# Optimization experiments

Measured on AMD Instinct MI355X. Metric: run time of the kernel, lower is better.

## Reference

```python
import jax, jax.numpy as jnp
import numpy as np

N_USERS = 100000
N_ITEMS = 50000
N_TOPICS = 1000
N_NODES = N_USERS + N_ITEMS + N_TOPICS
DIM = 64
LAYERS = 3
NNZ = 4000000
BATCH = 16384


def setup_inputs() -> dict:
    key = jax.random.key(0)
    ks = jax.random.split(key, 8)
    user_w = jax.random.normal(ks[0], (N_USERS, DIM), dtype=jnp.float32) * 0.1
    item_w = jax.random.normal(ks[1], (N_ITEMS, DIM), dtype=jnp.float32) * 0.1
    topic_w = jax.random.normal(ks[2], (N_TOPICS, DIM), dtype=jnp.float32) * 0.1
    vals = jax.random.uniform(ks[3], (NNZ,), dtype=jnp.float32)
    row = jax.random.randint(ks[4], (NNZ,), 0, N_NODES, dtype=jnp.int32)
    col = jax.random.randint(ks[5], (NNZ,), 0, N_NODES, dtype=jnp.int32)
    users = jax.random.randint(ks[6], (BATCH,), 0, N_USERS, dtype=jnp.int32)
    items = jax.random.randint(ks[7], (BATCH,), 0, N_ITEMS, dtype=jnp.int32)
    return {"user_w": user_w, "item_w": item_w, "topic_w": topic_w,
            "vals": vals, "row": row, "col": col,
            "users": users, "items": items}


def _spmm(vals, row, col, x):
    # y[r] = sum over edges e with row[e]==r of vals[e] * x[col[e]]
    msgs = vals[:, None] * x[col]  # [NNZ, DIM]
    return jax.ops.segment_sum(msgs, row, num_segments=N_NODES)


def reference(user_w, item_w, topic_w, vals, row, col, users, items):
    all_emb = jnp.concatenate([user_w, item_w, topic_w], axis=0)  # [N, D]
    acc = all_emb
    emb = all_emb
    for _ in range(LAYERS):
        emb = _spmm(vals, row, col, emb)
        acc = acc + emb
    out = acc / jnp.asarray(LAYERS + 1, dtype=acc.dtype)  # mean over stacked layers
    u = out[users]                       # [B, D] user rows
    i = out[N_USERS + items]             # [B, D] item rows (offset into node table)
    return jnp.sum(u * i, axis=1)        # [B]
```

## Files before the change

kernel.cpp:

```cpp
#include <hip/hip_runtime.h>
#include <hip/hip_fp16.h>

#define N_USERS 100000
#define N_ITEMS 50000
#define N_TOPICS 1000
#define N_NODES (N_USERS + N_ITEMS + N_TOPICS)
#define DIM 64
#define NNZ 4000000
#define BATCH 16384

#define BROWS 128
#define NB ((N_NODES + BROWS - 1) / BROWS)
#define NPART 256
#define CHUNK ((NNZ + NPART - 1) / NPART)
#define SUB 7813
#define SEGCAP 4608

#define QSCALE 16384.0f
#define QINV   6.103515625e-05f

#define CONCAT_TOTAL (N_NODES * (DIM / 4))
#define CONCAT_BLOCKS ((CONCAT_TOTAL + 1023) / 1024)
#define BINIT_TOTAL (2 * BATCH * (DIM / 4))
#define BINIT_BLOCKS ((BINIT_TOTAL + 1023) / 1024)

__global__ void __launch_bounds__(1024)
phase0(const float4* __restrict__ uw,
       const float4* __restrict__ iw,
       const float4* __restrict__ tw,
       const int* __restrict__ row,
       const int* __restrict__ users,
       const int* __restrict__ items,
       __half2* __restrict__ x0,
       float4* __restrict__ accb,
       int* __restrict__ hcnt,
       int* __restrict__ sync) {
    __shared__ int h[NB];
    const int blk = blockIdx.x;
    const int t = threadIdx.x;
    if (blk < NPART) {
        if (blk == 0 && t == 0) *sync = 0;
        for (int i = t; i < NB; i += 1024) h[i] = 0;
        __syncthreads();
        int e0 = blk * CHUNK;
        int e1 = e0 + CHUNK; if (e1 > NNZ) e1 = NNZ;
        for (int e = e0 + t; e < e1; e += 1024) {
            int r = __builtin_nontemporal_load(&row[e]);
            atomicAdd(&h[r >> 7], 1);
        }
        __syncthreads();
        int* dst = hcnt + (size_t)blk * NB;
        for (int i = t; i < NB; i += 1024) dst[i] = h[i];
    } else if (blk < NPART + CONCAT_BLOCKS) {
        int tid = (blk - NPART) * 1024 + t;
        if (tid >= CONCAT_TOTAL) return;
        int node = tid >> 4;
        int q = tid & 15;
        float4 v;
        if (node < N_USERS)                v = uw[node * 16 + q];
        else if (node < N_USERS + N_ITEMS) v = iw[(node - N_USERS) * 16 + q];
        else                               v = tw[(node - N_USERS - N_ITEMS) * 16 + q];
        x0[tid * 2]     = __floats2half2_rn(v.x, v.y);
        x0[tid * 2 + 1] = __floats2half2_rn(v.z, v.w);
    } else {
        int tid = (blk - NPART - CONCAT_BLOCKS) * 1024 + t;
        if (tid >= BINIT_TOTAL) return;
        int r = tid >> 4;
        int q = tid & 15;
        float4 v;
        if (r < BATCH) v = uw[(size_t)users[r] * 16 + q];
        else           v = iw[(size_t)items[r - BATCH] * 16 + q];
        accb[tid] = v;
    }
}

__global__ void __launch_bounds__(256)
part_scanAB(int* __restrict__ hcnt,
            int* __restrict__ bcnt,
            int* __restrict__ bptr,
            int* __restrict__ rowptr,
            int* __restrict__ sync) {
    const int t = threadIdx.x;
    const int lane = t & 63;
    const int wid = t >> 6;
    int b = blockIdx.x * 4 + wid;
    int carry = 0;
    for (int base = 0; base < NPART; base += 64) {
        int g = base + lane;
        int v = hcnt[(size_t)g * NB + b];
        int x = v;
        #pragma unroll
        for (int off = 1; off < 64; off <<= 1) {
            int y = __shfl_up(x, off, 64);
            if (lane >= off) x += y;
        }
        int tot = __shfl(x, 63, 64);
        hcnt[(size_t)g * NB + b] = carry + x - v;
        carry += tot;
    }
    if (lane == 0) bcnt[b] = carry;
    __syncthreads();
    __threadfence();
    __shared__ int lastFlag;
    if (t == 0) lastFlag = (atomicAdd(sync, 1) == (int)gridDim.x - 1);
    __syncthreads();
    if (!lastFlag) return;

    __shared__ int wsum[4];
    __shared__ int carry_s;
    if (t == 0) carry_s = 0;
    __syncthreads();
    for (int base = 0; base < NB; base += 256) {
        int i = base + t;
        int v = (i < NB) ? bcnt[i] : 0;
        int x = v;
        #pragma unroll
        for (int off = 1; off < 64; off <<= 1) {
            int y = __shfl_up(x, off, 64);
            if (lane >= off) x += y;
        }
        if (lane == 63) wsum[wid] = x;
        __syncthreads();
        int wbase = 0;
        for (int w = 0; w < wid; ++w) wbase += wsum[w];
        int excl = carry_s + wbase + (x - v);
        if (i < NB) bptr[i] = excl;
        __syncthreads();
        if (t == 255) carry_s = excl + v;
        __syncthreads();
    }
    if (t == 0) { bptr[NB] = NNZ; rowptr[N_NODES] = NNZ; }
}

__global__ void __launch_bounds__(1024)
part_scatter(const int* __restrict__ row,
             const int* __restrict__ col,
             const float* __restrict__ vals,
             const int* __restrict__ hcnt,
             const int* __restrict__ bptr,
             int2* __restrict__ cvtmp) {
    __shared__ int2 sorted[SUB];
    __shared__ unsigned short bktSorted[SUB];
    __shared__ int cnt_s[NB];
    __shared__ int cur_s[NB];
    __shared__ int gcur[NB];
    __shared__ int wsum[16];
    __shared__ int carry_s;
    const int g = blockIdx.x;
    const int t = threadIdx.x;
    const int lane = t & 63;
    const int wid = t >> 6;
    const int* hoff = hcnt + (size_t)g * NB;
    for (int i = t; i < NB; i += 1024) gcur[i] = bptr[i] + hoff[i];
    int e0 = g * CHUNK;
    int e1 = e0 + CHUNK; if (e1 > NNZ) e1 = NNZ;

    for (int s0 = e0; s0 < e1; s0 += SUB) {
        int n = e1 - s0; if (n > SUB) n = SUB;
        for (int i = t; i < NB; i += 1024) cnt_s[i] = 0;
        if (t == 0) carry_s = 0;
        __syncthreads();
        for (int j = t; j < n; j += 1024) {
            int r = __builtin_nontemporal_load(&row[s0 + j]);
            atomicAdd(&cnt_s[r >> 7], 1);
        }
        __syncthreads();
        for (int base = 0; base < NB; base += 1024) {
            int i = base + t;
            int v = (i < NB) ? cnt_s[i] : 0;
            int x = v;
            #pragma unroll
            for (int off = 1; off < 64; off <<= 1) {
                int y = __shfl_up(x, off, 64);
                if (lane >= off) x += y;
            }
            if (lane == 63) wsum[wid] = x;
            __syncthreads();
            int wbase = 0;
            for (int w = 0; w < wid; ++w) wbase += wsum[w];
            int excl = carry_s + wbase + (x - v);
            if (i < NB) cur_s[i] = excl;
            __syncthreads();
            if (t == 1023) carry_s = excl + v;
            __syncthreads();
        }
        for (int j = t; j < n; j += 1024) {
            int r = __builtin_nontemporal_load(&row[s0 + j]);
            int c = __builtin_nontemporal_load(&col[s0 + j]);
            float v = __builtin_nontemporal_load(&vals[s0 + j]);
            int b = r >> 7;
            int p = atomicAdd(&cur_s[b], 1);
            sorted[p] = make_int2(((r & (BROWS - 1)) << 18) | c, __float_as_int(v));
            bktSorted[p] = (unsigned short)b;
        }
        __syncthreads();
        for (int j = t; j < n; j += 1024) {
            int b = bktSorted[j];
            int lb = cur_s[b] - cnt_s[b];
            cvtmp[gcur[b] + (j - lb)] = sorted[j];
        }
        __syncthreads();
        for (int i = t; i < NB; i += 1024) gcur[i] += cnt_s[i];
        __syncthreads();
    }
}

__global__ void __launch_bounds__(512)
bucket_sort(const int* __restrict__ bptr,
            const long long* __restrict__ cvtmp,
            unsigned int* __restrict__ cv,
            int* __restrict__ rowptr) {
    __shared__ int2 seg[SEGCAP];
    __shared__ int cnt[BROWS];
    __shared__ int cur[BROWS];
    const int t = threadIdx.x;
    const int b = blockIdx.x;
    const int beg = bptr[b];
    const int end = bptr[b + 1];
    const int n = end - beg;

    for (int i = t; i < BROWS; i += 512) cnt[i] = 0;
    const bool lds_path = (n <= SEGCAP);

    if (lds_path) {
        for (int j = t; j < n; j += 512) {
            long long e = __builtin_nontemporal_load(&cvtmp[beg + j]);
            seg[j] = make_int2((int)e, (int)(e >> 32));
        }
    }
    __syncthreads();

    if (lds_path) {
        for (int j = t; j < n; j += 512)
            atomicAdd(&cnt[(seg[j].x >> 18) & (BROWS - 1)], 1);
    } else {
        for (int j = beg + t; j < end; j += 512) {
            long long e = cvtmp[j];
            atomicAdd(&cnt[((int)e >> 18) & (BROWS - 1)], 1);
        }
    }
    __syncthreads();

    if (t < 64) {
        int lane = t;
        int v0 = cnt[lane];
        int v1 = cnt[64 + lane];
        int x0 = v0;
        #pragma unroll
        for (int off = 1; off < 64; off <<= 1) {
            int y = __shfl_up(x0, off, 64);
            if (lane >= off) x0 += y;
        }
        int tot0 = __shfl(x0, 63, 64);
        int x1 = v1;
        #pragma unroll
        for (int off = 1; off < 64; off <<= 1) {
            int y = __shfl_up(x1, off, 64);
            if (lane >= off) x1 += y;
        }
        x1 += tot0;
        int e0 = x0 - v0;
        int e1 = x1 - v1;
        cur[lane] = e0;
        cur[64 + lane] = e1;
        int rowbase = b * BROWS;
        if (rowbase + lane < N_NODES)      rowptr[rowbase + lane] = beg + e0;
        if (rowbase + 64 + lane < N_NODES) rowptr[rowbase + 64 + lane] = beg + e1;
    }
    __syncthreads();

    if (lds_path) {
        for (int j = t; j < n; j += 512) {
            int2 e = seg[j];
            int p = atomicAdd(&cur[(e.x >> 18) & (BROWS - 1)], 1);
            float v = __int_as_float(e.y);
            unsigned int qv = (unsigned int)(v * QSCALE + 0.5f);
            if (qv > 16383u) qv = 16383u;
            cv[beg + p] = (qv << 18) | (unsigned int)(e.x & 0x3FFFF);
        }
    } else {
        for (int j = beg + t; j < end; j += 512) {
            long long e = cvtmp[j];
            int lo = (int)e;
            float v = __int_as_float((int)(e >> 32));
            int p = atomicAdd(&cur[(lo >> 18) & (BROWS - 1)], 1);
            unsigned int qv = (unsigned int)(v * QSCALE + 0.5f);
            if (qv > 16383u) qv = 16383u;
            cv[beg + p] = (qv << 18) | (unsigned int)(lo & 0x3FFFF);
        }
    }
}

__global__ void spmm_csr(const int* __restrict__ rowptr,
                         const unsigned int* __restrict__ cv,
                         const __half2* __restrict__ x2,
                         __half2* __restrict__ y2) {
    int bucket = blockIdx.x >> 3;
    int sub = blockIdx.x & 7;
    int lane = threadIdx.x & 63;
    int grp = lane >> 4;
    int d = lane & 15;
    int r = bucket * BROWS + sub * 16 + (threadIdx.x >> 6) * 4 + grp;
    if (r >= N_NODES) return;
    const uint2* xv = (const uint2*)x2;
    int beg = rowptr[r];
    int end = rowptr[r + 1];
    float ax0 = 0.0f, ay0 = 0.0f, ax1 = 0.0f, ay1 = 0.0f;
    int j = beg;
    for (; j + 7 < end; j += 8) {
        unsigned int u[8];
        uint2 h[8];
        #pragma unroll
        for (int k = 0; k < 8; ++k) u[k] = cv[j + k];
        #pragma unroll
        for (int k = 0; k < 8; ++k) h[k] = xv[(size_t)(u[k] & 0x3FFFF) * 16 + d];
        #pragma unroll
        for (int k = 0; k < 8; ++k) {
            float v = (float)(u[k] >> 18) * QINV;
            __half2 h0, h1;
            __builtin_memcpy(&h0, &h[k].x, 4);
            __builtin_memcpy(&h1, &h[k].y, 4);
            float2 f0 = __half22float2(h0);
            float2 f1 = __half22float2(h1);
            ax0 = fmaf(v, f0.x, ax0); ay0 = fmaf(v, f0.y, ay0);
            ax1 = fmaf(v, f1.x, ax1); ay1 = fmaf(v, f1.y, ay1);
        }
    }
    for (; j + 3 < end; j += 4) {
        unsigned int u[4];
        uint2 h[4];
        #pragma unroll
        for (int k = 0; k < 4; ++k) u[k] = cv[j + k];
        #pragma unroll
        for (int k = 0; k < 4; ++k) h[k] = xv[(size_t)(u[k] & 0x3FFFF) * 16 + d];
        #pragma unroll
        for (int k = 0; k < 4; ++k) {
            float v = (float)(u[k] >> 18) * QINV;
            __half2 h0, h1;
            __builtin_memcpy(&h0, &h[k].x, 4);
            __builtin_memcpy(&h1, &h[k].y, 4);
            float2 f0 = __half22float2(h0);
            float2 f1 = __half22float2(h1);
            ax0 = fmaf(v, f0.x, ax0); ay0 = fmaf(v, f0.y, ay0);
            ax1 = fmaf(v, f1.x, ax1); ay1 = fmaf(v, f1.y, ay1);
        }
    }
    for (; j < end; ++j) {
        unsigned int u = cv[j];
        uint2 h = xv[(size_t)(u & 0x3FFFF) * 16 + d];
        float v = (float)(u >> 18) * QINV;
        __half2 h0, h1;
        __builtin_memcpy(&h0, &h.x, 4);
        __builtin_memcpy(&h1, &h.y, 4);
        float2 f0 = __half22float2(h0);
        float2 f1 = __half22float2(h1);
        ax0 = fmaf(v, f0.x, ax0); ay0 = fmaf(v, f0.y, ay0);
        ax1 = fmaf(v, f1.x, ax1); ay1 = fmaf(v, f1.y, ay1);
    }
    __half2 o0 = __floats2half2_rn(ax0, ay0);
    __half2 o1 = __floats2half2_rn(ax1, ay1);
    unsigned int w0, w1;
    __builtin_memcpy(&w0, &o0, 4);
    __builtin_memcpy(&w1, &o1, 4);
    unsigned long long ob = (unsigned long long)w0 |
                            ((unsigned long long)w1 << 32);
    __builtin_nontemporal_store(ob,
        (unsigned long long*)&y2[(size_t)r * 32 + 2 * d]);
}

__global__ void spmm_batch(const int* __restrict__ rowptr,
                           const unsigned int* __restrict__ cv,
                           const __half2* __restrict__ xA,
                           const __half2* __restrict__ xB,
                           const int* __restrict__ users,
                           const int* __restrict__ items,
                           float* __restrict__ accb) {
    int lane = threadIdx.x & 63;
    int grp = lane >> 4;
    int d = lane & 15;
    int b = blockIdx.x * 16 + (threadIdx.x >> 6) * 4 + grp;
    if (b >= 2 * BATCH) return;
    const uint2* xv = (const uint2*)xA;
    const uint2* xv1 = (const uint2*)xB;
    int r = (b < BATCH) ? users[b] : (N_USERS + items[b - BATCH]);
    int beg = rowptr[r];
    int end = rowptr[r + 1];
    uint2 tA = xv[(size_t)r * 16 + d];
    uint2 tB = xv1[(size_t)r * 16 + d];
    __half2 tA0, tA1, tB0, tB1;
    __builtin_memcpy(&tA0, &tA.x, 4);
    __builtin_memcpy(&tA1, &tA.y, 4);
    __builtin_memcpy(&tB0, &tB.x, 4);
    __builtin_memcpy(&tB1, &tB.y, 4);
    float2 fA0 = __half22float2(tA0), fA1 = __half22float2(tA1);
    float2 fB0 = __half22float2(tB0), fB1 = __half22float2(tB1);
    float ax0 = fA0.x + fB0.x, ay0 = fA0.y + fB0.y;
    float ax1 = fA1.x + fB1.x, ay1 = fA1.y + fB1.y;
    int j = beg;
    for (; j + 7 < end; j += 8) {
        unsigned int u[8];
        uint2 h[8];
        #pragma unroll
        for (int k = 0; k < 8; ++k) u[k] = cv[j + k];
        #pragma unroll
        for (int k = 0; k < 8; ++k) h[k] = xv[(size_t)(u[k] & 0x3FFFF) * 16 + d];
        #pragma unroll
        for (int k = 0; k < 8; ++k) {
            float v = (float)(u[k] >> 18) * QINV;
            __half2 h0, h1;
            __builtin_memcpy(&h0, &h[k].x, 4);
            __builtin_memcpy(&h1, &h[k].y, 4);
            float2 f0 = __half22float2(h0);
            float2 f1 = __half22float2(h1);
            ax0 = fmaf(v, f0.x, ax0); ay0 = fmaf(v, f0.y, ay0);
            ax1 = fmaf(v, f1.x, ax1); ay1 = fmaf(v, f1.y, ay1);
        }
    }
    for (; j + 3 < end; j += 4) {
        unsigned int u[4];
        uint2 h[4];
        #pragma unroll
        for (int k = 0; k < 4; ++k) u[k] = cv[j + k];
        #pragma unroll
        for (int k = 0; k < 4; ++k) h[k] = xv[(size_t)(u[k] & 0x3FFFF) * 16 + d];
        #pragma unroll
        for (int k = 0; k < 4; ++k) {
            float v = (float)(u[k] >> 18) * QINV;
            __half2 h0, h1;
            __builtin_memcpy(&h0, &h[k].x, 4);
            __builtin_memcpy(&h1, &h[k].y, 4);
            float2 f0 = __half22float2(h0);
            float2 f1 = __half22float2(h1);
            ax0 = fmaf(v, f0.x, ax0); ay0 = fmaf(v, f0.y, ay0);
            ax1 = fmaf(v, f1.x, ax1); ay1 = fmaf(v, f1.y, ay1);
        }
    }
    for (; j < end; ++j) {
        unsigned int u = cv[j];
        uint2 h = xv[(size_t)(u & 0x3FFFF) * 16 + d];
        float v = (float)(u >> 18) * QINV;
        __half2 h0, h1;
        __builtin_memcpy(&h0, &h.x, 4);
        __builtin_memcpy(&h1, &h.y, 4);
        float2 f0 = __half22float2(h0);
        float2 f1 = __half22float2(h1);
        ax0 = fmaf(v, f0.x, ax0); ay0 = fmaf(v, f0.y, ay0);
        ax1 = fmaf(v, f1.x, ax1); ay1 = fmaf(v, f1.y, ay1);
    }
    float4* a4 = (float4*)(accb + (size_t)b * 64 + 4 * d);
    float4 o = *a4;
    o.x += ax0; o.y += ay0; o.z += ax1; o.w += ay1;
    *a4 = o;
}

__global__ void final_dot(const float* __restrict__ accb,
                          float* __restrict__ out) {
    int b = blockIdx.x * 4 + (threadIdx.x >> 6);
    int lane = threadIdx.x & 63;
    if (b >= BATCH) return;
    float pu = accb[(size_t)b * 64 + lane];
    float pi = accb[(size_t)(BATCH + b) * 64 + lane];
    float p = pu * pi;
    #pragma unroll
    for (int off = 32; off > 0; off >>= 1)
        p += __shfl_down(p, off, 64);
    if (lane == 0) out[b] = p * (1.0f / 16.0f);
}

extern "C" void kernel_launch(void* const* d_in, const int* in_sizes, int n_in,
                              void* d_out, int out_size, void* d_ws, size_t ws_size,
                              hipStream_t stream) {
    const float* uw   = (const float*)d_in[0];
    const float* iw   = (const float*)d_in[1];
    const float* tw   = (const float*)d_in[2];
    const float* vals = (const float*)d_in[3];
    const int*   row  = (const int*)d_in[4];
    const int*   col  = (const int*)d_in[5];
    const int*   users= (const int*)d_in[6];
    const int*   items= (const int*)d_in[7];
    float* out = (float*)d_out;

    char* ws = (char*)d_ws;
    const size_t NODE_F = (size_t)N_NODES * DIM;
    __half* A     = (__half*)ws; ws += NODE_F * 2;
    __half* B     = (__half*)ws; ws += NODE_F * 2;
    float* ACCB   = (float*)ws;  ws += (size_t)2 * BATCH * DIM * 4;
    int*   bcnt   = (int*)ws;    ws += (size_t)NB * 4;
    int*   bptr   = (int*)ws;    ws += (size_t)(NB + 1) * 4;
    int*   rowptr = (int*)ws;    ws += (size_t)(N_NODES + 1) * 4;
    int*   hcnt   = (int*)ws;    ws += (size_t)NPART * NB * 4;
    int*   sync   = (int*)ws;    ws += 64;
    unsigned int* cv = (unsigned int*)ws; ws += (size_t)NNZ * 4;
    int2*  cvtmp  = (int2*)ws;   ws += (size_t)NNZ * 8;

    phase0<<<NPART + CONCAT_BLOCKS + BINIT_BLOCKS, 1024, 0, stream>>>(
        (const float4*)uw, (const float4*)iw, (const float4*)tw, row,
        users, items, (__half2*)A, (float4*)ACCB, hcnt, sync);

    part_scanAB<<<NB / 4, 256, 0, stream>>>(hcnt, bcnt, bptr, rowptr, sync);
    part_scatter<<<NPART, 1024, 0, stream>>>(row, col, vals, hcnt, bptr, cvtmp);
    bucket_sort<<<NB, 512, 0, stream>>>(bptr, (const long long*)cvtmp, cv, rowptr);

    const int spmm_blocks = NB * 8;
    spmm_csr<<<spmm_blocks, 256, 0, stream>>>(rowptr, cv, (const __half2*)A,
                                              (__half2*)B);
    spmm_csr<<<spmm_blocks, 256, 0, stream>>>(rowptr, cv, (const __half2*)B,
                                              (__half2*)A);
    spmm_batch<<<(2 * BATCH + 15) / 16, 256, 0, stream>>>(
        rowptr, cv, (const __half2*)A, (const __half2*)B, users, items, ACCB);

    final_dot<<<(BATCH + 3) / 4, 256, 0, stream>>>(ACCB, out);
}
```

Measured before the change: 394.3 us.

## Split scatter temp into key/quantized value arrays, stage rows in LDS, fold acc init

The edge value is quantized to 14 bits during the partition scatter, and the intermediate buffer becomes a 4-byte key array plus a 2-byte value array instead of 8-byte pairs. This cuts scatter write and bucket-sort read traffic. Row indices are staged in shared memory so the second pass does not reload them from global memory. The batch accumulator initialisation moves out of phase0 into spmm_batch, which now reads the original fp32 embedding directly and writes the result once instead of doing a read-modify-write. The cost is extra LDS use in part_scatter, which may lower occupancy.

```diff
diff --git a/kernel.cpp b/kernel.cpp
--- a/kernel.cpp
+++ b/kernel.cpp
@@ -21,18 +21,13 @@
 
 #define CONCAT_TOTAL (N_NODES * (DIM / 4))
 #define CONCAT_BLOCKS ((CONCAT_TOTAL + 1023) / 1024)
-#define BINIT_TOTAL (2 * BATCH * (DIM / 4))
-#define BINIT_BLOCKS ((BINIT_TOTAL + 1023) / 1024)
 
 __global__ void __launch_bounds__(1024)
 phase0(const float4* __restrict__ uw,
        const float4* __restrict__ iw,
        const float4* __restrict__ tw,
        const int* __restrict__ row,
-       const int* __restrict__ users,
-       const int* __restrict__ items,
        __half2* __restrict__ x0,
-       float4* __restrict__ accb,
        int* __restrict__ hcnt,
        int* __restrict__ sync) {
     __shared__ int h[NB];
@@ -51,7 +46,7 @@
         __syncthreads();
         int* dst = hcnt + (size_t)blk * NB;
         for (int i = t; i < NB; i += 1024) dst[i] = h[i];
-    } else if (blk < NPART + CONCAT_BLOCKS) {
+    } else {
         int tid = (blk - NPART) * 1024 + t;
         if (tid >= CONCAT_TOTAL) return;
         int node = tid >> 4;
@@ -62,15 +57,6 @@
         else                               v = tw[(node - N_USERS - N_ITEMS) * 16 + q];
         x0[tid * 2]     = __floats2half2_rn(v.x, v.y);
         x0[tid * 2 + 1] = __floats2half2_rn(v.z, v.w);
-    } else {
-        int tid = (blk - NPART - CONCAT_BLOCKS) * 1024 + t;
-        if (tid >= BINIT_TOTAL) return;
-        int r = tid >> 4;
-        int q = tid & 15;
-        float4 v;
-        if (r < BATCH) v = uw[(size_t)users[r] * 16 + q];
-        else           v = iw[(size_t)items[r - BATCH] * 16 + q];
-        accb[tid] = v;
     }
 }
 
@@ -138,8 +124,11 @@
              const float* __restrict__ vals,
              const int* __restrict__ hcnt,
              const int* __restrict__ bptr,
-             int2* __restrict__ cvtmp) {
-    __shared__ int2 sorted[SUB];
+             unsigned int* __restrict__ cvK,
+             unsigned short* __restrict__ cvV) {
+    __shared__ int rStage[SUB];
+    __shared__ unsigned int sortedK[SUB];
+    __shared__ unsigned short sortedV[SUB];
     __shared__ unsigned short bktSorted[SUB];
     __shared__ int cnt_s[NB];
     __shared__ int cur_s[NB];
@@ -162,6 +151,7 @@
         __syncthreads();
         for (int j = t; j < n; j += 1024) {
             int r = __builtin_nontemporal_load(&row[s0 + j]);
+            rStage[j] = r;
             atomicAdd(&cnt_s[r >> 7], 1);
         }
         __syncthreads();
@@ -185,19 +175,24 @@
             __syncthreads();
         }
         for (int j = t; j < n; j += 1024) {
-            int r = __builtin_nontemporal_load(&row[s0 + j]);
+            int r = rStage[j];
             int c = __builtin_nontemporal_load(&col[s0 + j]);
             float v = __builtin_nontemporal_load(&vals[s0 + j]);
+            unsigned int qv = (unsigned int)(v * QSCALE + 0.5f);
+            if (qv > 16383u) qv = 16383u;
             int b = r >> 7;
             int p = atomicAdd(&cur_s[b], 1);
-            sorted[p] = make_int2(((r & (BROWS - 1)) << 18) | c, __float_as_int(v));
+            sortedK[p] = (unsigned int)(((r & (BROWS - 1)) << 18) | c);
+            sortedV[p] = (unsigned short)qv;
             bktSorted[p] = (unsigned short)b;
         }
         __syncthreads();
         for (int j = t; j < n; j += 1024) {
             int b = bktSorted[j];
             int lb = cur_s[b] - cnt_s[b];
-            cvtmp[gcur[b] + (j - lb)] = sorted[j];
+            int dst = gcur[b] + (j - lb);
+            cvK[dst] = sortedK[j];
+            cvV[dst] = sortedV[j];
         }
         __syncthreads();
         for (int i = t; i < NB; i += 1024) gcur[i] += cnt_s[i];
@@ -207,10 +202,12 @@
 
 __global__ void __launch_bounds__(512)
 bucket_sort(const int* __restrict__ bptr,
-            const long long* __restrict__ cvtmp,
+            const unsigned int* __restrict__ cvK,
+            const unsigned short* __restrict__ cvV,
             unsigned int* __restrict__ cv,
             int* __restrict__ rowptr) {
-    __shared__ int2 seg[SEGCAP];
+    __shared__ unsigned int segK[SEGCAP];
+    __shared__ unsigned short segV[SEGCAP];
     __shared__ int cnt[BROWS];
     __shared__ int cur[BROWS];
     const int t = threadIdx.x;
@@ -224,20 +221,18 @@
 
     if (lds_path) {
         for (int j = t; j < n; j += 512) {
-            long long e = __builtin_nontemporal_load(&cvtmp[beg + j]);
-            seg[j] = make_int2((int)e, (int)(e >> 32));
+            segK[j] = __builtin_nontemporal_load(&cvK[beg + j]);
+            segV[j] = __builtin_nontemporal_load(&cvV[beg + j]);
         }
     }
     __syncthreads();
 
     if (lds_path) {
         for (int j = t; j < n; j += 512)
-            atomicAdd(&cnt[(seg[j].x >> 18) & (BROWS - 1)], 1);
+            atomicAdd(&cnt[(segK[j] >> 18) & (BROWS - 1)], 1);
     } else {
-        for (int j = beg + t; j < end; j += 512) {
-            long long e = cvtmp[j];
-            atomicAdd(&cnt[((int)e >> 18) & (BROWS - 1)], 1);
-        }
+        for (int j = beg + t; j < end; j += 512)
+            atomicAdd(&cnt[(cvK[j] >> 18) & (BROWS - 1)], 1);
     }
     __syncthreads();
 
@@ -271,22 +266,16 @@
 
     if (lds_path) {
         for (int j = t; j < n; j += 512) {
-            int2 e = seg[j];
-            int p = atomicAdd(&cur[(e.x >> 18) & (BROWS - 1)], 1);
-            float v = __int_as_float(e.y);
-            unsigned int qv = (unsigned int)(v * QSCALE + 0.5f);
-            if (qv > 16383u) qv = 16383u;
-            cv[beg + p] = (qv << 18) | (unsigned int)(e.x & 0x3FFFF);
+            unsigned int k = segK[j];
+            int p = atomicAdd(&cur[(k >> 18) & (BROWS - 1)], 1);
+            cv[beg + p] = ((unsigned int)segV[j] << 18) | (k & 0x3FFFF);
         }
     } else {
         for (int j = beg + t; j < end; j += 512) {
-            long long e = cvtmp[j];
-            int lo = (int)e;
-            float v = __int_as_float((int)(e >> 32));
-            int p = atomicAdd(&cur[(lo >> 18) & (BROWS - 1)], 1);
-            unsigned int qv = (unsigned int)(v * QSCALE + 0.5f);
-            if (qv > 16383u) qv = 16383u;
-            cv[beg + p] = (qv << 18) | (unsigned int)(lo & 0x3FFFF);
+            unsigned int k = cvK[j];
+            unsigned int qv = cvV[j];
+            int p = atomicAdd(&cur[(k >> 18) & (BROWS - 1)], 1);
+            cv[beg + p] = (qv << 18) | (k & 0x3FFFF);
         }
     }
 }
@@ -372,6 +361,8 @@
                            const unsigned int* __restrict__ cv,
                            const __half2* __restrict__ xA,
                            const __half2* __restrict__ xB,
+                           const float4* __restrict__ uw,
+                           const float4* __restrict__ iw,
                            const int* __restrict__ users,
                            const int* __restrict__ items,
                            float* __restrict__ accb) {
@@ -382,7 +373,10 @@
     if (b >= 2 * BATCH) return;
     const uint2* xv = (const uint2*)xA;
     const uint2* xv1 = (const uint2*)xB;
-    int r = (b < BATCH) ? users[b] : (N_USERS + items[b - BATCH]);
+    int r;
+    float4 x0;
+    if (b < BATCH) { int u = users[b]; r = u; x0 = uw[(size_t)u * 16 + d]; }
+    else { int it = items[b - BATCH]; r = N_USERS + it; x0 = iw[(size_t)it * 16 + d]; }
     int beg = rowptr[r];
     int end = rowptr[r + 1];
     uint2 tA = xv[(size_t)r * 16 + d];
@@ -394,8 +388,8 @@
     __builtin_memcpy(&tB1, &tB.y, 4);
     float2 fA0 = __half22float2(tA0), fA1 = __half22float2(tA1);
     float2 fB0 = __half22float2(tB0), fB1 = __half22float2(tB1);
-    float ax0 = fA0.x + fB0.x, ay0 = fA0.y + fB0.y;
-    float ax1 = fA1.x + fB1.x, ay1 = fA1.y + fB1.y;
+    float ax0 = x0.x + fA0.x + fB0.x, ay0 = x0.y + fA0.y + fB0.y;
+    float ax1 = x0.z + fA1.x + fB1.x, ay1 = x0.w + fA1.y + fB1.y;
     int j = beg;
     for (; j + 7 < end; j += 8) {
         unsigned int u[8];
@@ -448,9 +442,7 @@
         ax1 = fmaf(v, f1.x, ax1); ay1 = fmaf(v, f1.y, ay1);
     }
     float4* a4 = (float4*)(accb + (size_t)b * 64 + 4 * d);
-    float4 o = *a4;
-    o.x += ax0; o.y += ay0; o.z += ax1; o.w += ay1;
-    *a4 = o;
+    *a4 = make_float4(ax0, ay0, ax1, ay1);
 }
 
 __global__ void final_dot(const float* __restrict__ accb,
@@ -490,16 +482,17 @@
     int*   rowptr = (int*)ws;    ws += (size_t)(N_NODES + 1) * 4;
     int*   hcnt   = (int*)ws;    ws += (size_t)NPART * NB * 4;
     int*   sync   = (int*)ws;    ws += 64;
-    unsigned int* cv = (unsigned int*)ws; ws += (size_t)NNZ * 4;
-    int2*  cvtmp  = (int2*)ws;   ws += (size_t)NNZ * 8;
-
-    phase0<<<NPART + CONCAT_BLOCKS + BINIT_BLOCKS, 1024, 0, stream>>>(
+    unsigned int* cv  = (unsigned int*)ws;  ws += (size_t)NNZ * 4;
+    unsigned int* cvK = (unsigned int*)ws;  ws += (size_t)NNZ * 4;
+    unsigned short* cvV = (unsigned short*)ws; ws += (size_t)NNZ * 2;
+
+    phase0<<<NPART + CONCAT_BLOCKS, 1024, 0, stream>>>(
         (const float4*)uw, (const float4*)iw, (const float4*)tw, row,
-        users, items, (__half2*)A, (float4*)ACCB, hcnt, sync);
+        (__half2*)A, hcnt, sync);
 
     part_scanAB<<<NB / 4, 256, 0, stream>>>(hcnt, bcnt, bptr, rowptr, sync);
-    part_scatter<<<NPART, 1024, 0, stream>>>(row, col, vals, hcnt, bptr, cvtmp);
-    bucket_sort<<<NB, 512, 0, stream>>>(bptr, (const long long*)cvtmp, cv, rowptr);
+    part_scatter<<<NPART, 1024, 0, stream>>>(row, col, vals, hcnt, bptr, cvK, cvV);
+    bucket_sort<<<NB, 512, 0, stream>>>(bptr, cvK, cvV, cv, rowptr);
 
     const int spmm_blocks = NB * 8;
     spmm_csr<<<spmm_blocks, 256, 0, stream>>>(rowptr, cv, (const __half2*)A,
@@ -507,7 +500,8 @@
     spmm_csr<<<spmm_blocks, 256, 0, stream>>>(rowptr, cv, (const __half2*)B,
                                               (__half2*)A);
     spmm_batch<<<(2 * BATCH + 15) / 16, 256, 0, stream>>>(
-        rowptr, cv, (const __half2*)A, (const __half2*)B, users, items, ACCB);
+        rowptr, cv, (const __half2*)A, (const __half2*)B,
+        (const float4*)uw, (const float4*)iw, users, items, ACCB);
 
     final_dot<<<(BATCH + 3) / 4, 256, 0, stream>>>(ACCB, out);
 }
```

New measurement: 393.5 us. Within noise of the previous version (-0.2%).
